# Kernel tuning notes

Measured on AMD Instinct MI355X. Metric: run time of the kernel, lower is better.

Reference implementation:

```python
import jax, jax.numpy as jnp
import numpy as np

B, C_ATT, C_VAL = 1, 64, 64
T, H, W = 40, 32, 32
HW = H * W
TOPK = 10
TEMP = 0.07
NEIGHBOR_RANGE = 24  # circle mode -> radius = 24 // 2
NON_MASK_LEN = 1     # first frame is not masked
NEG_INF = -1e30


def _spatial_neighbor_circle(h, w, neighbor_range):
    """Circle-mode spatial neighbor mask, (h*w, h*w) bool."""
    radius = neighbor_range // 2
    gy, gx = jnp.meshgrid(jnp.arange(h, dtype=jnp.float32),
                          jnp.arange(w, dtype=jnp.float32), indexing='ij')
    dy = gy[:, :, None, None] - gy[None, None, :, :]
    dx = gx[:, :, None, None] - gx[None, None, :, :]
    dist = jnp.sqrt(dy * dy + dx * dx)
    return (dist < radius).reshape(h * w, h * w)


def setup_inputs() -> dict:
    key0 = jax.random.key(0)
    k1, k2, k3 = jax.random.split(key0, 3)
    query = jax.random.normal(k1, (B, C_ATT, H, W), dtype=jnp.float32)
    key = jax.random.normal(k2, (B, C_ATT, T, H, W), dtype=jnp.float32)
    value = jax.random.normal(k3, (B, C_VAL, T, H, W), dtype=jnp.float32)
    mask = _spatial_neighbor_circle(H, W, NEIGHBOR_RANGE)  # (HW, HW) bool
    return {"query": query, "key": key, "value": value, "mask": mask}


def _l2_normalize(x, axis, eps=1e-12):
    # matches F.normalize(p=2): x / max(||x||, eps)
    n = jnp.sqrt(jnp.sum(x * x, axis=axis, keepdims=True))
    return x / jnp.maximum(n, eps)


def reference(query, key, value, mask):
    # normalize along channel dim
    q = _l2_normalize(query, axis=1).reshape(B, C_ATT, HW)          # (B,C,Q)
    k = _l2_normalize(key, axis=1).reshape(B, C_ATT, T * HW)        # (B,C,K)
    v = value.reshape(B, C_VAL, T * HW)                             # (B,Cv,K)

    # affinity over all keys vs all queries (chunking in the original is a
    # pure memory optimization; the math per query column is identical)
    aff = jnp.einsum('bck,bcq->bkq', k, q) / TEMP                   # (B,K,Q)

    # build full mask: first NON_MASK_LEN frames fully visible, remaining
    # frames restricted to the spatial-neighbor circle
    tiled = jnp.tile(mask, (T - NON_MASK_LEN, 1))                   # ((T-nm)*HW, Q)
    full_mask = jnp.concatenate(
        [jnp.ones((NON_MASK_LEN * HW, HW), dtype=bool), tiled], axis=0)  # (K,Q)
    aff = jnp.where(full_mask[None], aff, NEG_INF)

    # top-k over the key dimension, per query
    aff_qk = jnp.swapaxes(aff, 1, 2)                                # (B,Q,K)
    top_vals, top_idx = jax.lax.top_k(aff_qk, TOPK)                 # (B,Q,topk)
    weights = jax.nn.softmax(top_vals, axis=-1)                     # (B,Q,topk)

    # gather top-k values: (B,Cv,Q,topk)
    gathered = jnp.take_along_axis(v[:, :, None, :], top_idx[:, None, :, :], axis=3)
    out = jnp.einsum('bcqk,bqk->bcq', gathered, weights)            # (B,Cv,Q)
    return out.reshape(B, C_VAL, H, W)
```

## Files before the change

kernel.cpp:

```cpp
#include <hip/hip_runtime.h>
#include <hip/hip_bf16.h>
#include <float.h>

#define HWQ   1024
#define NK    40960
#define NCH   64
#define NTOP  10
#define NJOBS 82
#define NPART (NJOBS * NTOP)
#define R2    144
#define CAP   48
#define TSCALE 14.2857142857142857f
#define LOSCL  4.8828125e-4f

typedef _Float16 f16x8 __attribute__((ext_vector_type(8)));
typedef float    f32x4 __attribute__((ext_vector_type(4)));
typedef unsigned long long u64;
typedef unsigned int       u32;

__device__ inline float bf16bits_to_f32(unsigned short u) {
    union { u32 i; float f; } z; z.i = ((u32)u) << 16; return z.f;
}
__device__ inline unsigned short f32_to_bf16bits(float x) {
    __hip_bfloat16 b = __float2bfloat16(x);
    return *(unsigned short*)&b;
}

__device__ inline int sniff_fp32(const unsigned short* __restrict__ raw) {
    const int lane = threadIdx.x & 63;
    const int e = (raw[lane] >> 7) & 0xFF;
    const u64 m = __ballot(e < 100 || e > 133);
    return __popcll(m) > 16;
}

__device__ inline u64 pack_vi(float val, int kidx) {
    const u32 b = __float_as_uint(val);
    const u32 u = b ^ (u32)(((int)b >> 31) | (int)0x80000000);
    return ((u64)u << 16) | (u32)(0xFFFF - kidx);
}
__device__ inline float unpack_val(u64 p) {
    const u32 u = (u32)(p >> 16);
    const u32 b = u ^ (~((u32)((int)u >> 31)) | 0x80000000u);
    return __uint_as_float(b);
}
__device__ inline int unpack_idx(u64 p) { return 0xFFFF - (int)(p & 0xFFFF); }

__device__ inline void ins10(u64* v, u64 pk) {
#pragma unroll
    for (int j = NTOP - 1; j >= 1; --j) {
        const bool gj = pk > v[j];
        const bool gp = pk > v[j - 1];
        v[j] = gj ? (gp ? v[j - 1] : pk) : v[j];
    }
    if (pk > v[0]) v[0] = pk;
}

__global__ __launch_bounds__(64) void prep_all(
    const void* __restrict__ qin_, const void* __restrict__ kin_,
    const void* __restrict__ vin_,
    f16x8* __restrict__ kh, f16x8* __restrict__ kl,
    f16x8* __restrict__ qh, f16x8* __restrict__ ql,
    unsigned short* __restrict__ vt)
{
    const int isf  = sniff_fp32((const unsigned short*)kin_);
    const int bid  = blockIdx.x;
    const int lane = threadIdx.x;

    if (bid < NK / 64) {
        const int key = bid * 64 + lane;
        float kv[NCH];
        if (isf) {
            const float* p = (const float*)kin_;
#pragma unroll
            for (int c = 0; c < NCH; ++c) kv[c] = p[c * NK + key];
        } else {
            const __hip_bfloat16* p = (const __hip_bfloat16*)kin_;
#pragma unroll
            for (int c = 0; c < NCH; ++c) kv[c] = __bfloat162float(p[c * NK + key]);
        }
        float s = 0.f;
#pragma unroll
        for (int c = 0; c < NCH; ++c) s = fmaf(kv[c], kv[c], s);
        const float rn = 1.0f / fmaxf(sqrtf(s), 1e-12f);

        const int tb = (key >> 4) * 128 + (key & 15);
#pragma unroll
        for (int blk = 0; blk < 8; ++blk) {
            f16x8 h, l;
#pragma unroll
            for (int j = 0; j < 8; ++j) {
                const float x = kv[blk * 8 + j] * rn;
                const _Float16 hh = (_Float16)x;
                h[j] = hh;
                l[j] = (_Float16)((x - (float)hh) * 2048.0f);
            }
            kh[tb + blk * 16] = h;
            kl[tb + blk * 16] = l;
        }

        if (isf) {
            const float* p = (const float*)vin_;
#pragma unroll
            for (int c = 0; c < NCH; ++c)
                vt[(size_t)key * NCH + c] = f32_to_bf16bits(p[c * NK + key]);
        } else {
            const unsigned short* p = (const unsigned short*)vin_;
#pragma unroll
            for (int c = 0; c < NCH; ++c) vt[(size_t)key * NCH + c] = p[c * NK + key];
        }
    } else {
        const int q = (bid - NK / 64) * 64 + lane;
        float qv[NCH];
        if (isf) {
            const float* p = (const float*)qin_;
#pragma unroll
            for (int c = 0; c < NCH; ++c) qv[c] = p[c * HWQ + q];
        } else {
            const __hip_bfloat16* p = (const __hip_bfloat16*)qin_;
#pragma unroll
            for (int c = 0; c < NCH; ++c) qv[c] = __bfloat162float(p[c * HWQ + q]);
        }
        float s = 0.f;
#pragma unroll
        for (int c = 0; c < NCH; ++c) s = fmaf(qv[c], qv[c], s);
        const float rn = 1.0f / fmaxf(sqrtf(s), 1e-12f);

        const int tb = (q >> 4) * 128 + (q & 15);
#pragma unroll
        for (int blk = 0; blk < 8; ++blk) {
            f16x8 h, l;
#pragma unroll
            for (int j = 0; j < 8; ++j) {
                const float x = qv[blk * 8 + j] * rn;
                const _Float16 hh = (_Float16)x;
                h[j] = hh;
                l[j] = (_Float16)((x - (float)hh) * 2048.0f);
            }
            qh[tb + blk * 16] = h;
            ql[tb + blk * 16] = l;
        }
    }
}

__device__ inline void quad_merge_store(
    u64 (*sm)[16][NTOP], int lane, u64* out10)
{
    int p0 = 0, p1 = 0, p2 = 0, p3 = 0;
#pragma unroll
    for (int r = 0; r < NTOP; ++r) {
        const u64 h0 = sm[0][lane][p0], h1 = sm[1][lane][p1];
        const u64 h2 = sm[2][lane][p2], h3 = sm[3][lane][p3];
        u64 m = h0; int sel = 0;
        if (h1 > m) { m = h1; sel = 1; }
        if (h2 > m) { m = h2; sel = 2; }
        if (h3 > m) { m = h3; sel = 3; }
        out10[r] = m;
        p0 += (sel == 0); p1 += (sel == 1); p2 += (sel == 2); p3 += (sel == 3);
    }
}

__global__ __launch_bounds__(128) void attn_f0(
    const f16x8* __restrict__ kh, const f16x8* __restrict__ kl,
    const f16x8* __restrict__ qh, const f16x8* __restrict__ ql,
    u64* __restrict__ pv, float* __restrict__ th)
{
    __shared__ u64 sm[2][4][16][NTOP];

    const int tid  = threadIdx.x;
    const int w    = tid >> 6;
    const int lane = tid & 63;
    const int quad = lane >> 4;
    const int n    = lane & 15;

    const int t   = blockIdx.x * 2 + w;
    const int job = blockIdx.y;

    const int qb = t * 128 + n;
    const f16x8 bh0 = qh[qb + (0 + quad) * 16];
    const f16x8 bh1 = qh[qb + (4 + quad) * 16];
    const f16x8 bl0 = ql[qb + (0 + quad) * 16];
    const f16x8 bl1 = ql[qb + (4 + quad) * 16];

    u64 v[NTOP];
#pragma unroll
    for (int j = 0; j < NTOP; ++j) v[j] = 0ull;

    const int start = job * 16, end = start + 16;
    int base = start * 128 + n;
    f16x8 nah0 = kh[base + (0 + quad) * 16], nah1 = kh[base + (4 + quad) * 16];
    f16x8 nal0 = kl[base + (0 + quad) * 16], nal1 = kl[base + (4 + quad) * 16];

    for (int kt = start; kt < end; ++kt) {
        const f16x8 ah0 = nah0, ah1 = nah1, al0 = nal0, al1 = nal1;
        const int ktn = (kt + 1 < end) ? kt + 1 : kt;
        base = ktn * 128 + n;
        nah0 = kh[base + (0 + quad) * 16]; nah1 = kh[base + (4 + quad) * 16];
        nal0 = kl[base + (0 + quad) * 16]; nal1 = kl[base + (4 + quad) * 16];

        f32x4 accH = {0.f,0.f,0.f,0.f}, accL0 = {0.f,0.f,0.f,0.f}, accL1 = {0.f,0.f,0.f,0.f};
        accH  = __builtin_amdgcn_mfma_f32_16x16x32_f16(ah0, bh0, accH, 0, 0, 0);
        accH  = __builtin_amdgcn_mfma_f32_16x16x32_f16(ah1, bh1, accH, 0, 0, 0);
        accL0 = __builtin_amdgcn_mfma_f32_16x16x32_f16(ah0, bl0, accL0, 0, 0, 0);
        accL0 = __builtin_amdgcn_mfma_f32_16x16x32_f16(al0, bh0, accL0, 0, 0, 0);
        accL1 = __builtin_amdgcn_mfma_f32_16x16x32_f16(ah1, bl1, accL1, 0, 0, 0);
        accL1 = __builtin_amdgcn_mfma_f32_16x16x32_f16(al1, bh1, accL1, 0, 0, 0);

        const int key0 = kt * 16 + quad * 4;
#pragma unroll
        for (int r = 0; r < 4; ++r) {
            const float val = fmaf(accL0[r] + accL1[r], LOSCL, accH[r]);
            const u64 pk = pack_vi(val, key0 + r);
            if (pk > v[NTOP - 1]) ins10(v, pk);
        }
    }

#pragma unroll
    for (int j = 0; j < NTOP; ++j) sm[w][quad][n][j] = v[j];
    __syncthreads();

    if (lane < 16) {
        u64 out10[NTOP];
        quad_merge_store(sm[w], lane, out10);
        const int q = t * 16 + lane;
#pragma unroll
        for (int r = 0; r < NTOP; ++r) pv[(size_t)q * NPART + job * NTOP + r] = out10[r];
        th[q * 4 + job] = unpack_val(out10[9]);
    }
}

__global__ __launch_bounds__(128) void attn_masked(
    const f16x8* __restrict__ kh, const f16x8* __restrict__ kl,
    const f16x8* __restrict__ qh, const f16x8* __restrict__ ql,
    const float* __restrict__ th, u64* __restrict__ pv)
{
    __shared__ u64 cand[2][16][CAP];
    __shared__ int cnt[2][16];

    const int tid  = threadIdx.x;
    const int w    = tid >> 6;
    const int lane = tid & 63;
    const int quad = lane >> 4;
    const int n    = lane & 15;

    const int qy   = blockIdx.x;
    const int t    = qy * 2 + w;
    const int yy   = blockIdx.y;
    const int f    = (yy >> 1) + 1;
    const int half = yy & 1;
    const int qx   = (t & 1) * 16 + n;
    const int q    = t * 16 + n;

    if (tid < 32) cnt[tid >> 4][tid & 15] = 0;
    __syncthreads();

    const float theta = fmaxf(fmaxf(th[q * 4 + 0], th[q * 4 + 1]),
                              fmaxf(th[q * 4 + 2], th[q * 4 + 3]));

    const int qb = t * 128 + n;
    const f16x8 bh0 = qh[qb + (0 + quad) * 16];
    const f16x8 bh1 = qh[qb + (4 + quad) * 16];
    const f16x8 bl0 = ql[qb + (0 + quad) * 16];
    const f16x8 bl1 = ql[qb + (4 + quad) * 16];

    const int rlo  = (qy > 11) ? qy - 11 : 0;
    const int rhi  = (qy < 20) ? qy + 11 : 31;
    const int mid  = (rlo + rhi + 1) >> 1;
    const int row0 = half ? mid : rlo;
    const int row1 = half ? rhi + 1 : mid;
    const int start = f * 64 + 2 * row0;
    const int end   = f * 64 + 2 * row1;

    int base = start * 128 + n;
    f16x8 nah0 = kh[base + (0 + quad) * 16], nah1 = kh[base + (4 + quad) * 16];
    f16x8 nal0 = kl[base + (0 + quad) * 16], nal1 = kl[base + (4 + quad) * 16];

    for (int kt = start; kt < end; ++kt) {
        const f16x8 ah0 = nah0, ah1 = nah1, al0 = nal0, al1 = nal1;
        const int ktn = (kt + 1 < end) ? kt + 1 : kt;
        base = ktn * 128 + n;
        nah0 = kh[base + (0 + quad) * 16]; nah1 = kh[base + (4 + quad) * 16];
        nal0 = kl[base + (0 + quad) * 16]; nal1 = kl[base + (4 + quad) * 16];

        f32x4 accH = {0.f,0.f,0.f,0.f}, accL0 = {0.f,0.f,0.f,0.f}, accL1 = {0.f,0.f,0.f,0.f};
        accH  = __builtin_amdgcn_mfma_f32_16x16x32_f16(ah0, bh0, accH, 0, 0, 0);
        accH  = __builtin_amdgcn_mfma_f32_16x16x32_f16(ah1, bh1, accH, 0, 0, 0);
        accL0 = __builtin_amdgcn_mfma_f32_16x16x32_f16(ah0, bl0, accL0, 0, 0, 0);
        accL0 = __builtin_amdgcn_mfma_f32_16x16x32_f16(al0, bh0, accL0, 0, 0, 0);
        accL1 = __builtin_amdgcn_mfma_f32_16x16x32_f16(ah1, bl1, accL1, 0, 0, 0);
        accL1 = __builtin_amdgcn_mfma_f32_16x16x32_f16(al1, bh1, accL1, 0, 0, 0);

        const int ky   = (kt >> 1) & 31;
        const int dy   = ky - qy;
        const int rem  = R2 - dy * dy;
        const int d0   = (kt & 1) * 16 + quad * 4 - qx;
        const int key0 = kt * 16 + quad * 4;
#pragma unroll
        for (int r = 0; r < 4; ++r) {
            const float val = fmaf(accL0[r] + accL1[r], LOSCL, accH[r]);
            const int dx = d0 + r;
            if (val > theta && dx * dx < rem) {
                const int pos = atomicAdd(&cnt[w][n], 1);
                if (pos < CAP) cand[w][n][pos] = pack_vi(val, key0 + r);
            }
        }
    }

    __syncthreads();
    if (lane < 16) {
        const int c = min(cnt[w][lane], CAP);
        u64 v[NTOP];
#pragma unroll
        for (int j = 0; j < NTOP; ++j) v[j] = 0ull;
        for (int e = 0; e < c; ++e) {
            const u64 pk = cand[w][lane][e];
            if (pk > v[NTOP - 1]) ins10(v, pk);
        }
        const int qq  = t * 16 + lane;
        const int job = 4 + (f - 1) * 2 + half;
#pragma unroll
        for (int r = 0; r < NTOP; ++r)
            pv[(size_t)qq * NPART + (size_t)job * NTOP + r] = v[r];
    }
}

__global__ __launch_bounds__(64) void finalize_kernel(
    const u64* __restrict__ pv, const unsigned short* __restrict__ vt,
    const unsigned short* __restrict__ kin_raw, void* __restrict__ out_)
{
    const int isf  = sniff_fp32(kin_raw);
    const int q    = blockIdx.x;
    const int lane = threadIdx.x;

    u64 lv[13];
#pragma unroll
    for (int e = 0; e < 13; ++e) {
        const int idx = e * 64 + lane;
        lv[e] = (idx < NPART) ? pv[(size_t)q * NPART + idx] : 0ull;
    }

    float wv[NTOP]; int wi[NTOP];
#pragma unroll
    for (int r = 0; r < NTOP; ++r) {
        u64 m = lv[0];
#pragma unroll
        for (int e = 1; e < 13; ++e) if (lv[e] > m) m = lv[e];
#pragma unroll
        for (int off = 32; off >= 1; off >>= 1) {
            const u32 lo = (u32)m, hi = (u32)(m >> 32);
            const u32 lo2 = (u32)__shfl_xor((int)lo, off);
            const u32 hi2 = (u32)__shfl_xor((int)hi, off);
            const u64 o = ((u64)hi2 << 32) | lo2;
            if (o > m) m = o;
        }
#pragma unroll
        for (int e = 0; e < 13; ++e) if (lv[e] == m) lv[e] = 0ull;
        wv[r] = unpack_val(m); wi[r] = unpack_idx(m);
    }

    float ww[NTOP]; float wsum = 0.f;
#pragma unroll
    for (int r = 0; r < NTOP; ++r) { ww[r] = expf((wv[r] - wv[0]) * TSCALE); wsum += ww[r]; }
    const float inv = 1.0f / wsum;

    float acc = 0.f;
#pragma unroll
    for (int r = 0; r < NTOP; ++r)
        acc += ww[r] * bf16bits_to_f32(vt[(size_t)wi[r] * NCH + lane]);
    const float res = acc * inv;

    if (isf) ((float*)out_)[lane * HWQ + q] = res;
    else     ((__hip_bfloat16*)out_)[lane * HWQ + q] = __float2bfloat16(res);
}

extern "C" void kernel_launch(void* const* d_in, const int* in_sizes, int n_in,
                              void* d_out, int out_size, void* d_ws, size_t ws_size,
                              hipStream_t stream)
{
    const void* qin = d_in[0];
    const void* kin = d_in[1];
    const void* vin = d_in[2];

    char* w = (char*)d_ws;
    f16x8*          kh  = (f16x8*)(w);
    f16x8*          kl  = (f16x8*)(w + 5242880);
    f16x8*          qhv = (f16x8*)(w + 10485760);
    f16x8*          qlv = (f16x8*)(w + 10616832);
    unsigned short* vt  = (unsigned short*)(w + 10747904);
    u64*            pv  = (u64*)(w + 15990784);
    float*          th  = (float*)(w + 22708224);

    prep_all<<<NK / 64 + HWQ / 64, 64, 0, stream>>>(qin, kin, vin, kh, kl, qhv, qlv, vt);
    attn_f0<<<dim3(32, 4), 128, 0, stream>>>(kh, kl, qhv, qlv, pv, th);
    attn_masked<<<dim3(32, 78), 128, 0, stream>>>(kh, kl, qhv, qlv, th, pv);
    finalize_kernel<<<HWQ, 64, 0, stream>>>(pv, vt, (const unsigned short*)kin, d_out);
}
```

Baseline: 150.0 us.

## Restructure prep, frame-0 and masked attention kernels with wider work per block

```diff
diff --git a/kernel.cpp b/kernel.cpp
--- a/kernel.cpp
+++ b/kernel.cpp
@@ -6,7 +6,7 @@
 #define NK    40960
 #define NCH   64
 #define NTOP  10
-#define NJOBS 82
+#define NJOBS 47
 #define NPART (NJOBS * NTOP)
 #define R2    144
 #define CAP   48
@@ -15,6 +15,7 @@
 
 typedef _Float16 f16x8 __attribute__((ext_vector_type(8)));
 typedef float    f32x4 __attribute__((ext_vector_type(4)));
+typedef unsigned short us8 __attribute__((ext_vector_type(8)));
 typedef unsigned long long u64;
 typedef unsigned int       u32;
 
@@ -33,16 +34,18 @@
     return __popcll(m) > 16;
 }
 
-__device__ inline u64 pack_vi(float val, int kidx) {
-    const u32 b = __float_as_uint(val);
-    const u32 u = b ^ (u32)(((int)b >> 31) | (int)0x80000000);
-    return ((u64)u << 16) | (u32)(0xFFFF - kidx);
-}
-__device__ inline float unpack_val(u64 p) {
-    const u32 u = (u32)(p >> 16);
+__device__ inline u32 ord32(float v) {
+    const u32 b = __float_as_uint(v);
+    return b ^ (u32)(((int)b >> 31) | (int)0x80000000);
+}
+__device__ inline float unpack_ord32(u32 u) {
     const u32 b = u ^ (~((u32)((int)u >> 31)) | 0x80000000u);
     return __uint_as_float(b);
 }
+__device__ inline u64 pack_vi(float val, int kidx) {
+    return ((u64)ord32(val) << 16) | (u32)(0xFFFF - kidx);
+}
+__device__ inline float unpack_val(u64 p) { return unpack_ord32((u32)(p >> 16)); }
 __device__ inline int unpack_idx(u64 p) { return 0xFFFF - (int)(p & 0xFFFF); }
 
 __device__ inline void ins10(u64* v, u64 pk) {
@@ -55,89 +58,106 @@
     if (pk > v[0]) v[0] = pk;
 }
 
-__global__ __launch_bounds__(64) void prep_all(
+__global__ __launch_bounds__(256) void prep_all(
     const void* __restrict__ qin_, const void* __restrict__ kin_,
     const void* __restrict__ vin_,
     f16x8* __restrict__ kh, f16x8* __restrict__ kl,
     f16x8* __restrict__ qh, f16x8* __restrict__ ql,
-    unsigned short* __restrict__ vt)
-{
-    const int isf  = sniff_fp32((const unsigned short*)kin_);
-    const int bid  = blockIdx.x;
-    const int lane = threadIdx.x;
+    unsigned short* __restrict__ vt, u32* __restrict__ thmax)
+{
+    const int isf = sniff_fp32((const unsigned short*)kin_);
+    const int bid = blockIdx.x;
+    const int tid = threadIdx.x;
+    const int cg  = tid & 3;
+    const int c0  = cg * 16;
+
+    if (bid == 655) {
+        ((u32*)thmax)[tid * 4 + 0] = 0; ((u32*)thmax)[tid * 4 + 1] = 0;
+        ((u32*)thmax)[tid * 4 + 2] = 0; ((u32*)thmax)[tid * 4 + 3] = 0;
+    }
 
     if (bid < NK / 64) {
-        const int key = bid * 64 + lane;
-        float kv[NCH];
+        const int key = bid * 64 + (tid >> 2);
+        float x[16];
         if (isf) {
             const float* p = (const float*)kin_;
 #pragma unroll
-            for (int c = 0; c < NCH; ++c) kv[c] = p[c * NK + key];
+            for (int i = 0; i < 16; ++i) x[i] = p[(c0 + i) * NK + key];
         } else {
             const __hip_bfloat16* p = (const __hip_bfloat16*)kin_;
 #pragma unroll
-            for (int c = 0; c < NCH; ++c) kv[c] = __bfloat162float(p[c * NK + key]);
+            for (int i = 0; i < 16; ++i) x[i] = __bfloat162float(p[(c0 + i) * NK + key]);
         }
         float s = 0.f;
 #pragma unroll
-        for (int c = 0; c < NCH; ++c) s = fmaf(kv[c], kv[c], s);
+        for (int i = 0; i < 16; ++i) s = fmaf(x[i], x[i], s);
+        s += __shfl_xor(s, 1); s += __shfl_xor(s, 2);
         const float rn = 1.0f / fmaxf(sqrtf(s), 1e-12f);
 
         const int tb = (key >> 4) * 128 + (key & 15);
 #pragma unroll
-        for (int blk = 0; blk < 8; ++blk) {
+        for (int b2 = 0; b2 < 2; ++b2) {
             f16x8 h, l;
 #pragma unroll
-            for (int j = 0; j < 8; ++j) {
-                const float x = kv[blk * 8 + j] * rn;
-                const _Float16 hh = (_Float16)x;
-                h[j] = hh;
-                l[j] = (_Float16)((x - (float)hh) * 2048.0f);
+            for (int jj = 0; jj < 8; ++jj) {
+                const float xv = x[b2 * 8 + jj] * rn;
+                const _Float16 hh = (_Float16)xv;
+                h[jj] = hh;
+                l[jj] = (_Float16)((xv - (float)hh) * 2048.0f);
             }
-            kh[tb + blk * 16] = h;
-            kl[tb + blk * 16] = l;
-        }
-
+            kh[tb + (cg * 2 + b2) * 16] = h;
+            kl[tb + (cg * 2 + b2) * 16] = l;
+        }
+
+        unsigned short vv[16];
         if (isf) {
             const float* p = (const float*)vin_;
 #pragma unroll
-            for (int c = 0; c < NCH; ++c)
-                vt[(size_t)key * NCH + c] = f32_to_bf16bits(p[c * NK + key]);
+            for (int i = 0; i < 16; ++i) vv[i] = f32_to_bf16bits(p[(c0 + i) * NK + key]);
         } else {
             const unsigned short* p = (const unsigned short*)vin_;
 #pragma unroll
-            for (int c = 0; c < NCH; ++c) vt[(size_t)key * NCH + c] = p[c * NK + key];
+            for (int i = 0; i < 16; ++i) vv[i] = p[(c0 + i) * NK + key];
+        }
+        us8* dst = (us8*)(vt + (size_t)key * NCH + c0);
+#pragma unroll
+        for (int b2 = 0; b2 < 2; ++b2) {
+            us8 o;
+#pragma unroll
+            for (int e = 0; e < 8; ++e) o[e] = vv[b2 * 8 + e];
+            dst[b2] = o;
         }
     } else {
-        const int q = (bid - NK / 64) * 64 + lane;
-        float qv[NCH];
+        const int q = (bid - NK / 64) * 64 + (tid >> 2);
+        float x[16];
         if (isf) {
             const float* p = (const float*)qin_;
 #pragma unroll
-            for (int c = 0; c < NCH; ++c) qv[c] = p[c * HWQ + q];
+            for (int i = 0; i < 16; ++i) x[i] = p[(c0 + i) * HWQ + q];
         } else {
             const __hip_bfloat16* p = (const __hip_bfloat16*)qin_;
 #pragma unroll
-            for (int c = 0; c < NCH; ++c) qv[c] = __bfloat162float(p[c * HWQ + q]);
+            for (int i = 0; i < 16; ++i) x[i] = __bfloat162float(p[(c0 + i) * HWQ + q]);
         }
         float s = 0.f;
 #pragma unroll
-        for (int c = 0; c < NCH; ++c) s = fmaf(qv[c], qv[c], s);
+        for (int i = 0; i < 16; ++i) s = fmaf(x[i], x[i], s);
+        s += __shfl_xor(s, 1); s += __shfl_xor(s, 2);
         const float rn = 1.0f / fmaxf(sqrtf(s), 1e-12f);
 
         const int tb = (q >> 4) * 128 + (q & 15);
 #pragma unroll
-        for (int blk = 0; blk < 8; ++blk) {
+        for (int b2 = 0; b2 < 2; ++b2) {
             f16x8 h, l;
 #pragma unroll
-            for (int j = 0; j < 8; ++j) {
-                const float x = qv[blk * 8 + j] * rn;
-                const _Float16 hh = (_Float16)x;
-                h[j] = hh;
-                l[j] = (_Float16)((x - (float)hh) * 2048.0f);
+            for (int jj = 0; jj < 8; ++jj) {
+                const float xv = x[b2 * 8 + jj] * rn;
+                const _Float16 hh = (_Float16)xv;
+                h[jj] = hh;
+                l[jj] = (_Float16)((xv - (float)hh) * 2048.0f);
             }
-            qh[tb + blk * 16] = h;
-            ql[tb + blk * 16] = l;
+            qh[tb + (cg * 2 + b2) * 16] = h;
+            ql[tb + (cg * 2 + b2) * 16] = l;
         }
     }
 }
@@ -162,7 +182,7 @@
 __global__ __launch_bounds__(128) void attn_f0(
     const f16x8* __restrict__ kh, const f16x8* __restrict__ kl,
     const f16x8* __restrict__ qh, const f16x8* __restrict__ ql,
-    u64* __restrict__ pv, float* __restrict__ th)
+    u64* __restrict__ pv, u32* __restrict__ thmax)
 {
     __shared__ u64 sm[2][4][16][NTOP];
 
@@ -176,34 +196,41 @@
     const int job = blockIdx.y;
 
     const int qb = t * 128 + n;
-    const f16x8 bh0 = qh[qb + (0 + quad) * 16];
+    const f16x8 bh0 = qh[qb + quad * 16];
     const f16x8 bh1 = qh[qb + (4 + quad) * 16];
-    const f16x8 bl0 = ql[qb + (0 + quad) * 16];
+    const f16x8 bl0 = ql[qb + quad * 16];
     const f16x8 bl1 = ql[qb + (4 + quad) * 16];
 
     u64 v[NTOP];
 #pragma unroll
-    for (int j = 0; j < NTOP; ++j) v[j] = 0ull;
-
-    const int start = job * 16, end = start + 16;
-    int base = start * 128 + n;
-    f16x8 nah0 = kh[base + (0 + quad) * 16], nah1 = kh[base + (4 + quad) * 16];
-    f16x8 nal0 = kl[base + (0 + quad) * 16], nal1 = kl[base + (4 + quad) * 16];
+    for (int jj = 0; jj < NTOP; ++jj) v[jj] = 0ull;
+
+    const int start = job * 8, end = start + 8;
+    const int loff = (n + quad * 16) * 16;
+    const char* ph = (const char*)kh + (size_t)start * 2048 + loff;
+    const char* pl = (const char*)kl + (size_t)start * 2048 + loff;
+
+    f16x8 Ah0 = *(const f16x8*)(ph);
+    f16x8 Ah1 = *(const f16x8*)(ph + 1024);
+    f16x8 Al0 = *(const f16x8*)(pl);
+    f16x8 Al1 = *(const f16x8*)(pl + 1024);
 
     for (int kt = start; kt < end; ++kt) {
-        const f16x8 ah0 = nah0, ah1 = nah1, al0 = nal0, al1 = nal1;
-        const int ktn = (kt + 1 < end) ? kt + 1 : kt;
-        base = ktn * 128 + n;
-        nah0 = kh[base + (0 + quad) * 16]; nah1 = kh[base + (4 + quad) * 16];
-        nal0 = kl[base + (0 + quad) * 16]; nal1 = kl[base + (4 + quad) * 16];
+        const size_t adv = (kt + 1 < end) ? 2048 : 0;
+        const char* nh = ph + adv;
+        const char* nl = pl + adv;
+        const f16x8 Bh0 = *(const f16x8*)(nh);
+        const f16x8 Bh1 = *(const f16x8*)(nh + 1024);
+        const f16x8 Bl0 = *(const f16x8*)(nl);
+        const f16x8 Bl1 = *(const f16x8*)(nl + 1024);
 
         f32x4 accH = {0.f,0.f,0.f,0.f}, accL0 = {0.f,0.f,0.f,0.f}, accL1 = {0.f,0.f,0.f,0.f};
-        accH  = __builtin_amdgcn_mfma_f32_16x16x32_f16(ah0, bh0, accH, 0, 0, 0);
-        accH  = __builtin_amdgcn_mfma_f32_16x16x32_f16(ah1, bh1, accH, 0, 0, 0);
-        accL0 = __builtin_amdgcn_mfma_f32_16x16x32_f16(ah0, bl0, accL0, 0, 0, 0);
-        accL0 = __builtin_amdgcn_mfma_f32_16x16x32_f16(al0, bh0, accL0, 0, 0, 0);
-        accL1 = __builtin_amdgcn_mfma_f32_16x16x32_f16(ah1, bl1, accL1, 0, 0, 0);
-        accL1 = __builtin_amdgcn_mfma_f32_16x16x32_f16(al1, bh1, accL1, 0, 0, 0);
+        accH  = __builtin_amdgcn_mfma_f32_16x16x32_f16(Ah0, bh0, accH, 0, 0, 0);
+        accH  = __builtin_amdgcn_mfma_f32_16x16x32_f16(Ah1, bh1, accH, 0, 0, 0);
+        accL0 = __builtin_amdgcn_mfma_f32_16x16x32_f16(Ah0, bl0, accL0, 0, 0, 0);
+        accL0 = __builtin_amdgcn_mfma_f32_16x16x32_f16(Al0, bh0, accL0, 0, 0, 0);
+        accL1 = __builtin_amdgcn_mfma_f32_16x16x32_f16(Ah1, bl1, accL1, 0, 0, 0);
+        accL1 = __builtin_amdgcn_mfma_f32_16x16x32_f16(Al1, bh1, accL1, 0, 0, 0);
 
         const int key0 = kt * 16 + quad * 4;
 #pragma unroll
@@ -212,10 +239,12 @@
             const u64 pk = pack_vi(val, key0 + r);
             if (pk > v[NTOP - 1]) ins10(v, pk);
         }
-    }
-
-#pragma unroll
-    for (int j = 0; j < NTOP; ++j) sm[w][quad][n][j] = v[j];
+        Ah0 = Bh0; Ah1 = Bh1; Al0 = Bl0; Al1 = Bl1;
+        ph = nh; pl = nl;
+    }
+
+#pragma unroll
+    for (int jj = 0; jj < NTOP; ++jj) sm[w][quad][n][jj] = v[jj];
     __syncthreads();
 
     if (lane < 16) {
@@ -224,17 +253,17 @@
         const int q = t * 16 + lane;
 #pragma unroll
         for (int r = 0; r < NTOP; ++r) pv[(size_t)q * NPART + job * NTOP + r] = out10[r];
-        th[q * 4 + job] = unpack_val(out10[9]);
+        atomicMax(&thmax[q], (u32)(out10[9] >> 16));
     }
 }
 
 __global__ __launch_bounds__(128) void attn_masked(
     const f16x8* __restrict__ kh, const f16x8* __restrict__ kl,
     const f16x8* __restrict__ qh, const f16x8* __restrict__ ql,
-    const float* __restrict__ th, u64* __restrict__ pv)
-{
-    __shared__ u64 cand[2][16][CAP];
-    __shared__ int cnt[2][16];
+    const u32* __restrict__ thmax, u64* __restrict__ pv)
+{
+    __shared__ u64 cand[32][CAP];
+    __shared__ int cnt[32];
 
     const int tid  = threadIdx.x;
     const int w    = tid >> 6;
@@ -242,81 +271,122 @@
     const int quad = lane >> 4;
     const int n    = lane & 15;
 
-    const int qy   = blockIdx.x;
-    const int t    = qy * 2 + w;
-    const int yy   = blockIdx.y;
-    const int f    = (yy >> 1) + 1;
-    const int half = yy & 1;
-    const int qx   = (t & 1) * 16 + n;
-    const int q    = t * 16 + n;
-
-    if (tid < 32) cnt[tid >> 4][tid & 15] = 0;
+    const int lin   = blockIdx.x;
+    const int j     = (lin & 7) * 156 + (lin >> 3);
+    const int fm1   = j >> 5;
+    const int qy    = j & 31;
+    const int frame = fm1 + 1;
+
+    if (tid < 32) cnt[tid] = 0;
     __syncthreads();
 
-    const float theta = fmaxf(fmaxf(th[q * 4 + 0], th[q * 4 + 1]),
-                              fmaxf(th[q * 4 + 2], th[q * 4 + 3]));
-
-    const int qb = t * 128 + n;
-    const f16x8 bh0 = qh[qb + (0 + quad) * 16];
-    const f16x8 bh1 = qh[qb + (4 + quad) * 16];
-    const f16x8 bl0 = ql[qb + (0 + quad) * 16];
-    const f16x8 bl1 = ql[qb + (4 + quad) * 16];
-
-    const int rlo  = (qy > 11) ? qy - 11 : 0;
-    const int rhi  = (qy < 20) ? qy + 11 : 31;
-    const int mid  = (rlo + rhi + 1) >> 1;
-    const int row0 = half ? mid : rlo;
-    const int row1 = half ? rhi + 1 : mid;
-    const int start = f * 64 + 2 * row0;
-    const int end   = f * 64 + 2 * row1;
-
-    int base = start * 128 + n;
-    f16x8 nah0 = kh[base + (0 + quad) * 16], nah1 = kh[base + (4 + quad) * 16];
-    f16x8 nal0 = kl[base + (0 + quad) * 16], nal1 = kl[base + (4 + quad) * 16];
-
-    for (int kt = start; kt < end; ++kt) {
-        const f16x8 ah0 = nah0, ah1 = nah1, al0 = nal0, al1 = nal1;
-        const int ktn = (kt + 1 < end) ? kt + 1 : kt;
-        base = ktn * 128 + n;
-        nah0 = kh[base + (0 + quad) * 16]; nah1 = kh[base + (4 + quad) * 16];
-        nal0 = kl[base + (0 + quad) * 16]; nal1 = kl[base + (4 + quad) * 16];
-
-        f32x4 accH = {0.f,0.f,0.f,0.f}, accL0 = {0.f,0.f,0.f,0.f}, accL1 = {0.f,0.f,0.f,0.f};
-        accH  = __builtin_amdgcn_mfma_f32_16x16x32_f16(ah0, bh0, accH, 0, 0, 0);
-        accH  = __builtin_amdgcn_mfma_f32_16x16x32_f16(ah1, bh1, accH, 0, 0, 0);
-        accL0 = __builtin_amdgcn_mfma_f32_16x16x32_f16(ah0, bl0, accL0, 0, 0, 0);
-        accL0 = __builtin_amdgcn_mfma_f32_16x16x32_f16(al0, bh0, accL0, 0, 0, 0);
-        accL1 = __builtin_amdgcn_mfma_f32_16x16x32_f16(ah1, bl1, accL1, 0, 0, 0);
-        accL1 = __builtin_amdgcn_mfma_f32_16x16x32_f16(al1, bh1, accL1, 0, 0, 0);
-
-        const int ky   = (kt >> 1) & 31;
-        const int dy   = ky - qy;
-        const int rem  = R2 - dy * dy;
-        const int d0   = (kt & 1) * 16 + quad * 4 - qx;
-        const int key0 = kt * 16 + quad * 4;
-#pragma unroll
-        for (int r = 0; r < 4; ++r) {
-            const float val = fmaf(accL0[r] + accL1[r], LOSCL, accH[r]);
-            const int dx = d0 + r;
-            if (val > theta && dx * dx < rem) {
-                const int pos = atomicAdd(&cnt[w][n], 1);
-                if (pos < CAP) cand[w][n][pos] = pack_vi(val, key0 + r);
+    const int q0 = qy * 32 + n;
+    const float theta0 = unpack_ord32(thmax[q0]);
+    const float theta1 = unpack_ord32(thmax[q0 + 16]);
+
+    const int qb = (qy * 2) * 128 + n;
+    const f16x8 b0h0 = qh[qb + quad * 16];
+    const f16x8 b0h1 = qh[qb + (4 + quad) * 16];
+    const f16x8 b0l0 = ql[qb + quad * 16];
+    const f16x8 b0l1 = ql[qb + (4 + quad) * 16];
+    const f16x8 b1h0 = qh[qb + 128 + quad * 16];
+    const f16x8 b1h1 = qh[qb + 128 + (4 + quad) * 16];
+    const f16x8 b1l0 = ql[qb + 128 + quad * 16];
+    const f16x8 b1l1 = ql[qb + 128 + (4 + quad) * 16];
+
+    const int rlo = (qy > 11) ? qy - 11 : 0;
+    const int rhi = (qy < 20) ? qy + 11 : 31;
+    const int mid = (rlo + rhi + 1) >> 1;
+    const int r0  = w ? mid : rlo;
+    const int r1  = w ? (rhi + 1) : mid;
+
+    const int loff = (n + quad * 16) * 16;
+    const char* ph = (const char*)kh + (size_t)(frame * 64 + 2 * r0) * 2048 + loff;
+    const char* pl = (const char*)kl + (size_t)(frame * 64 + 2 * r0) * 2048 + loff;
+
+    f16x8 Ahe0 = *(const f16x8*)(ph);
+    f16x8 Ahe1 = *(const f16x8*)(ph + 1024);
+    f16x8 Aho0 = *(const f16x8*)(ph + 2048);
+    f16x8 Aho1 = *(const f16x8*)(ph + 3072);
+    f16x8 Ale0 = *(const f16x8*)(pl);
+    f16x8 Ale1 = *(const f16x8*)(pl + 1024);
+    f16x8 Alo0 = *(const f16x8*)(pl + 2048);
+    f16x8 Alo1 = *(const f16x8*)(pl + 3072);
+
+    for (int row = r0; row < r1; ++row) {
+        const size_t adv = (row + 1 < r1) ? 4096 : 0;
+        const char* nh = ph + adv;
+        const char* nl = pl + adv;
+        const f16x8 Bhe0 = *(const f16x8*)(nh);
+        const f16x8 Bhe1 = *(const f16x8*)(nh + 1024);
+        const f16x8 Bho0 = *(const f16x8*)(nh + 2048);
+        const f16x8 Bho1 = *(const f16x8*)(nh + 3072);
+        const f16x8 Ble0 = *(const f16x8*)(nl);
+        const f16x8 Ble1 = *(const f16x8*)(nl + 1024);
+        const f16x8 Blo0 = *(const f16x8*)(nl + 2048);
+        const f16x8 Blo1 = *(const f16x8*)(nl + 3072);
+
+        const int dy = row - qy;
+        const int rem = R2 - dy * dy;
+        const int keyrow = frame * 1024 + row * 32;
+
+#pragma unroll
+        for (int p = 0; p < 2; ++p) {
+            const f16x8 ah0 = p ? Aho0 : Ahe0;
+            const f16x8 ah1 = p ? Aho1 : Ahe1;
+            const f16x8 al0 = p ? Alo0 : Ale0;
+            const f16x8 al1 = p ? Alo1 : Ale1;
+
+            f32x4 aH0 = {0.f,0.f,0.f,0.f}, aL00 = {0.f,0.f,0.f,0.f}, aL01 = {0.f,0.f,0.f,0.f};
+            f32x4 aH1 = {0.f,0.f,0.f,0.f}, aL10 = {0.f,0.f,0.f,0.f}, aL11 = {0.f,0.f,0.f,0.f};
+            aH0  = __builtin_amdgcn_mfma_f32_16x16x32_f16(ah0, b0h0, aH0, 0, 0, 0);
+            aH0  = __builtin_amdgcn_mfma_f32_16x16x32_f16(ah1, b0h1, aH0, 0, 0, 0);
+            aL00 = __builtin_amdgcn_mfma_f32_16x16x32_f16(ah0, b0l0, aL00, 0, 0, 0);
+            aL00 = __builtin_amdgcn_mfma_f32_16x16x32_f16(al0, b0h0, aL00, 0, 0, 0);
+            aL01 = __builtin_amdgcn_mfma_f32_16x16x32_f16(ah1, b0l1, aL01, 0, 0, 0);
+            aL01 = __builtin_amdgcn_mfma_f32_16x16x32_f16(al1, b0h1, aL01, 0, 0, 0);
+            aH1  = __builtin_amdgcn_mfma_f32_16x16x32_f16(ah0, b1h0, aH1, 0, 0, 0);
+            aH1  = __builtin_amdgcn_mfma_f32_16x16x32_f16(ah1, b1h1, aH1, 0, 0, 0);
+            aL10 = __builtin_amdgcn_mfma_f32_16x16x32_f16(ah0, b1l0, aL10, 0, 0, 0);
+            aL10 = __builtin_amdgcn_mfma_f32_16x16x32_f16(al0, b1h0, aL10, 0, 0, 0);
+            aL11 = __builtin_amdgcn_mfma_f32_16x16x32_f16(ah1, b1l1, aL11, 0, 0, 0);
+            aL11 = __builtin_amdgcn_mfma_f32_16x16x32_f16(al1, b1h1, aL11, 0, 0, 0);
+
+            const int kx0 = p * 16 + quad * 4;
+            const int key0 = keyrow + kx0;
+#pragma unroll
+            for (int r = 0; r < 4; ++r) {
+                const float v0 = fmaf(aL00[r] + aL01[r], LOSCL, aH0[r]);
+                const float v1 = fmaf(aL10[r] + aL11[r], LOSCL, aH1[r]);
+                const int dx0 = kx0 + r - n;
+                const int dx1 = dx0 - 16;
+                if (v0 > theta0 && dx0 * dx0 < rem) {
+                    const int pos = atomicAdd(&cnt[n], 1);
+                    if (pos < CAP) cand[n][pos] = pack_vi(v0, key0 + r);
+                }
+                if (v1 > theta1 && dx1 * dx1 < rem) {
+                    const int pos = atomicAdd(&cnt[16 + n], 1);
+                    if (pos < CAP) cand[16 + n][pos] = pack_vi(v1, key0 + r);
+                }
             }
         }
+        Ahe0 = Bhe0; Ahe1 = Bhe1; Aho0 = Bho0; Aho1 = Bho1;
+        Ale0 = Ble0; Ale1 = Ble1; Alo0 = Blo0; Alo1 = Blo1;
+        ph = nh; pl = nl;
     }
 
     __syncthreads();
-    if (lane < 16) {
-        const int c = min(cnt[w][lane], CAP);
+    if (tid < 32) {
+        const int c = min(cnt[tid], CAP);
         u64 v[NTOP];
 #pragma unroll
-        for (int j = 0; j < NTOP; ++j) v[j] = 0ull;
+        for (int e = 0; e < NTOP; ++e) v[e] = 0ull;
         for (int e = 0; e < c; ++e) {
-            const u64 pk = cand[w][lane][e];
+            const u64 pk = cand[tid][e];
             if (pk > v[NTOP - 1]) ins10(v, pk);
         }
-        const int qq  = t * 16 + lane;
-        const int job = 4 + (f - 1) * 2 + half;
+        const int qq  = qy * 32 + tid;
+        const int job = 8 + fm1;
 #pragma unroll
         for (int r = 0; r < NTOP; ++r)
             pv[(size_t)qq * NPART + (size_t)job * NTOP + r] = v[r];
@@ -331,9 +401,9 @@
     const int q    = blockIdx.x;
     const int lane = threadIdx.x;
 
-    u64 lv[13];
-#pragma unroll
-    for (int e = 0; e < 13; ++e) {
+    u64 lv[8];
+#pragma unroll
+    for (int e = 0; e < 8; ++e) {
         const int idx = e * 64 + lane;
         lv[e] = (idx < NPART) ? pv[(size_t)q * NPART + idx] : 0ull;
     }
@@ -343,7 +413,7 @@
     for (int r = 0; r < NTOP; ++r) {
         u64 m = lv[0];
 #pragma unroll
-        for (int e = 1; e < 13; ++e) if (lv[e] > m) m = lv[e];
+        for (int e = 1; e < 8; ++e) if (lv[e] > m) m = lv[e];
 #pragma unroll
         for (int off = 32; off >= 1; off >>= 1) {
             const u32 lo = (u32)m, hi = (u32)(m >> 32);
@@ -353,7 +423,7 @@
             if (o > m) m = o;
         }
 #pragma unroll
-        for (int e = 0; e < 13; ++e) if (lv[e] == m) lv[e] = 0ull;
+        for (int e = 0; e < 8; ++e) if (lv[e] == m) lv[e] = 0ull;
         wv[r] = unpack_val(m); wi[r] = unpack_idx(m);
     }
 
@@ -381,16 +451,16 @@
     const void* vin = d_in[2];
 
     char* w = (char*)d_ws;
-    f16x8*          kh  = (f16x8*)(w);
-    f16x8*          kl  = (f16x8*)(w + 5242880);
-    f16x8*          qhv = (f16x8*)(w + 10485760);
-    f16x8*          qlv = (f16x8*)(w + 10616832);
-    unsigned short* vt  = (unsigned short*)(w + 10747904);
-    u64*            pv  = (u64*)(w + 15990784);
-    float*          th  = (float*)(w + 22708224);
-
-    prep_all<<<NK / 64 + HWQ / 64, 64, 0, stream>>>(qin, kin, vin, kh, kl, qhv, qlv, vt);
-    attn_f0<<<dim3(32, 4), 128, 0, stream>>>(kh, kl, qhv, qlv, pv, th);
-    attn_masked<<<dim3(32, 78), 128, 0, stream>>>(kh, kl, qhv, qlv, th, pv);
+    f16x8*          kh    = (f16x8*)(w);
+    f16x8*          kl    = (f16x8*)(w + 5242880);
+    f16x8*          qhv   = (f16x8*)(w + 10485760);
+    f16x8*          qlv   = (f16x8*)(w + 10616832);
+    unsigned short* vt    = (unsigned short*)(w + 10747904);
+    u64*            pv    = (u64*)(w + 15990784);
+    u32*            thmax = (u32*)(w + 19841024);
+
+    prep_all<<<656, 256, 0, stream>>>(qin, kin, vin, kh, kl, qhv, qlv, vt, thmax);
+    attn_f0<<<dim3(32, 8), 128, 0, stream>>>(kh, kl, qhv, qlv, pv, thmax);
+    attn_masked<<<1248, 128, 0, stream>>>(kh, kl, qhv, qlv, thmax, pv);
     finalize_kernel<<<HWQ, 64, 0, stream>>>(pv, vt, (const unsigned short*)kin, d_out);
 }
```

Result: faster. 135.5 us (-9.7%).
